# Optimization experiments

Hardware: AMD Instinct MI355X
Metric: run time of the kernel (lower is better)

Reference implementation:

```python
import jax, jax.numpy as jnp
import numpy as np

H = 768; I = 3072; NH = 12; HD = H // NH; L = 2; V = 32000
N = 2048; NSUB = 8; SUBLEN = 256; WIDTH = 512; EPS = 1e-6


def rmsnorm(x, w):
    x32 = x.astype(jnp.float32)
    n = x32 * jax.lax.rsqrt(jnp.mean(x32 * x32, axis=-1, keepdims=True) + EPS)
    return (n * w).astype(x.dtype)


def fixed_pos_embedding(ages, dim):
    # inv_freq: [dim//2]; torch.linspace(0, 2, steps=dim//2)
    inv_freq = 1.0 / (10000.0 ** jnp.linspace(0.0, 2.0, dim // 2))
    t = ages[:, None] * inv_freq[None, :]              # [N, dim//2]
    # stack((s, s), -1).reshape -> duplicate each entry pairwise (interleaved)
    sin = jnp.repeat(jnp.sin(t), 2, axis=-1)[:, None, :]  # [N, 1, dim]
    cos = jnp.repeat(jnp.cos(t), 2, axis=-1)[:, None, :]
    return sin, cos


def apply_rope(x, sin, cos):
    # x: [N, heads, hd]; sin/cos: [N, 1, hd]
    x1 = x[..., 0::2]
    x2 = x[..., 1::2]
    rot = jnp.stack((-x2, x1), axis=-1).reshape(x.shape)
    return x * cos + rot * sin


def build_mask(subject_lengths, n):
    # block-diagonal (per subject) + causal local window of WIDTH
    csum = jnp.cumsum(subject_lengths)
    idx = jnp.arange(n)
    seg = jnp.searchsorted(csum, idx, side='right')   # subject id per token
    i = idx[:, None]; j = idx[None, :]
    same = seg[:, None] == seg[None, :]
    return same & (j <= i) & ((i - j) < WIDTH)        # [N, N] bool


def encoder_layer(x, time_data, sin, cos, mask, norm_w, W_in, W_out):
    h = rmsnorm(x, norm_w)
    all_time = jnp.concatenate((time_data, time_data ** 2), axis=-1)  # [N, 4]
    h = h.at[:, -all_time.shape[1]:].set(all_time.astype(h.dtype))
    t = h @ W_in                                      # [N, 2I + 3H]
    ff = t[:, : 2 * I]
    qkv = t[:, 2 * I:].reshape(-1, 3, NH, HD)
    q = apply_rope(qkv[:, 0], sin, cos)
    k = apply_rope(qkv[:, 1], sin, cos)
    v = qkv[:, 2]
    scores = jnp.einsum('qhd,khd->hqk', q, k) / jnp.sqrt(jnp.float32(HD))
    scores = jnp.where(mask[None, :, :], scores, -jnp.inf)
    probs = jax.nn.softmax(scores, axis=-1)
    attn = jnp.einsum('hqk,khd->qhd', probs, v).reshape(-1, H)
    x1, x2 = jnp.split(ff, 2, axis=-1)
    ffo = jax.nn.silu(x1) * x2                        # swiglu
    return jnp.concatenate((attn, ffo), axis=-1) @ W_out


def setup_inputs() -> dict:
    key = jax.random.key(0)
    ks = jax.random.split(key, 6)
    tokens = jax.random.randint(ks[0], (N,), 0, V)
    ages = jnp.sort(jax.random.uniform(ks[1], (N,), dtype=jnp.float32) * 100.0)
    time_data = jax.random.normal(ks[2], (N, 2), dtype=jnp.float32)
    subject_lengths = jnp.full((NSUB,), SUBLEN, dtype=jnp.int32)
    embed_table = jax.random.normal(ks[3], (V, H), dtype=jnp.float32) * 0.02
    in_norm_w = jnp.ones((H,), jnp.float32)
    out_norm_w = jnp.ones((H,), jnp.float32)
    layer_norm_w = jnp.ones((L, H), jnp.float32)
    layer_Win = jax.random.normal(ks[4], (L, H, 2 * I + 3 * H), dtype=jnp.float32) / np.sqrt(H)
    layer_Wout = jax.random.normal(ks[5], (L, H + I, H), dtype=jnp.float32) / np.sqrt(H + I)
    return dict(tokens=tokens, ages=ages, time_data=time_data,
                subject_lengths=subject_lengths, embed_table=embed_table,
                in_norm_w=in_norm_w, out_norm_w=out_norm_w,
                layer_norm_w=layer_norm_w, layer_Win=layer_Win, layer_Wout=layer_Wout)


def reference(tokens, ages, time_data, subject_lengths, embed_table,
              in_norm_w, out_norm_w, layer_norm_w, layer_Win, layer_Wout):
    x = embed_table[tokens]                           # [N, H]
    x = rmsnorm(x, in_norm_w)
    sin, cos = fixed_pos_embedding(ages, HD)
    mask = build_mask(subject_lengths, x.shape[0])
    for l in range(L):
        x = x + encoder_layer(x, time_data, sin, cos, mask,
                              layer_norm_w[l], layer_Win[l], layer_Wout[l])
    return rmsnorm(x, out_norm_w)
```

## Files before the change

### kernel.cpp

```cpp
#include <hip/hip_runtime.h>
#include <math.h>

typedef unsigned short ushort_t;
typedef float f32x4 __attribute__((ext_vector_type(4)));
typedef __bf16 bf16x8 __attribute__((ext_vector_type(8)));
typedef ushort_t u16x8 __attribute__((ext_vector_type(8)));

#define DEVFN __device__ __forceinline__

DEVFN ushort_t f2bf(float f) {
  unsigned int u = __float_as_uint(f);
  u += 0x7FFFu + ((u >> 16) & 1u);
  return (ushort_t)(u >> 16);
}
DEVFN float bf2f(ushort_t u) { return __uint_as_float((unsigned int)u << 16); }

DEVFN void gload(const ushort_t* src, char* dst) {
  __builtin_amdgcn_global_load_lds(
      (const __attribute__((address_space(1))) unsigned int*)src,
      (__attribute__((address_space(3))) unsigned int*)dst, 16, 0, 0);
}

#define N_TOK  2048
#define HDIM   768
#define TCOLS  8448
#define FFI    3072
#define NHEADS 12
#define HD     64
#define NSEG   8
#define SEGLEN 256
#define ABCOLS 3840
#define KSPLIT 5
#define KCHUNK 768

__global__ void transpose_all(const float* __restrict__ Win, const float* __restrict__ Wout,
                              ushort_t* __restrict__ winT, ushort_t* __restrict__ woutT) {
  __shared__ ushort_t tile[32][33];
  int id = blockIdx.x;
  const float* in; ushort_t* out; int R, C, tr, tc;
  if (id < 12672) {
    const int z = id / 6336; id -= z * 6336;
    R = HDIM; C = TCOLS;
    tc = (id % 264) * 32; tr = (id / 264) * 32;
    in = Win + (size_t)z * R * C; out = winT + (size_t)z * R * C;
  } else {
    id -= 12672;
    const int z = id / 2880; id -= z * 2880;
    R = ABCOLS; C = HDIM;
    tc = (id % 24) * 32; tr = (id / 24) * 32;
    in = Wout + (size_t)z * R * C; out = woutT + (size_t)z * R * C;
  }
  const int tx = threadIdx.x, ty = threadIdx.y;
#pragma unroll
  for (int i = 0; i < 4; ++i)
    tile[ty + i * 8][tx] = f2bf(in[(size_t)(tr + ty + i * 8) * C + tc + tx]);
  __syncthreads();
#pragma unroll
  for (int i = 0; i < 4; ++i)
    out[(size_t)(tc + ty + i * 8) * R + tr + tx] = tile[tx][ty + i * 8];
}

__global__ __launch_bounds__(256) void sincos_kernel(const float* __restrict__ ages,
                                                     float2* __restrict__ sctab) {
  const int n = blockIdx.x * 8 + (threadIdx.x >> 5), k = threadIdx.x & 31;
  const float e = (2.0f * (float)k) / 31.0f;
  const float inv = expf(-e * logf(10000.0f));
  const float t = ages[n] * inv;
  float2 cs; cs.x = cosf(t); cs.y = sinf(t);
  sctab[n * HD + 2 * k] = cs;
  sctab[n * HD + 2 * k + 1] = cs;
}

__global__ __launch_bounds__(256) void rms_init(
    const float* __restrict__ embed, const int* __restrict__ tokens,
    const float* __restrict__ in_nw, const float* __restrict__ layer_nw,
    const float* __restrict__ time_data,
    float* __restrict__ x, ushort_t* __restrict__ hbuf) {
  const int row = blockIdx.x;
  const float* src = embed + (size_t)tokens[row] * HDIM;
  __shared__ float part[4];
  float v[3]; float ss = 0.f;
#pragma unroll
  for (int i = 0; i < 3; ++i) { v[i] = src[threadIdx.x + i * 256]; ss += v[i] * v[i]; }
#pragma unroll
  for (int off = 1; off < 64; off <<= 1) ss += __shfl_xor(ss, off);
  if ((threadIdx.x & 63) == 0) part[threadIdx.x >> 6] = ss;
  __syncthreads();
  const float rs = rsqrtf((part[0] + part[1] + part[2] + part[3]) * (1.0f / HDIM) + 1e-6f);
  float y[3]; float ss2 = 0.f;
#pragma unroll
  for (int i = 0; i < 3; ++i) {
    const int c = threadIdx.x + i * 256;
    y[i] = v[i] * rs * in_nw[c];
    x[(size_t)row * HDIM + c] = y[i];
    ss2 += y[i] * y[i];
  }
#pragma unroll
  for (int off = 1; off < 64; off <<= 1) ss2 += __shfl_xor(ss2, off);
  __syncthreads();
  if ((threadIdx.x & 63) == 0) part[threadIdx.x >> 6] = ss2;
  __syncthreads();
  const float rs2 = rsqrtf((part[0] + part[1] + part[2] + part[3]) * (1.0f / HDIM) + 1e-6f);
#pragma unroll
  for (int i = 0; i < 3; ++i) {
    const int c = threadIdx.x + i * 256;
    float val = y[i] * rs2 * layer_nw[c];
    if (c >= HDIM - 4) {
      const float td = time_data[row * 2 + (c & 1)];
      val = (c >= HDIM - 2) ? td * td : td;
    }
    hbuf[(size_t)row * HDIM + c] = f2bf(val);
  }
}

__global__ __launch_bounds__(256) void rms_fused(
    const float* __restrict__ cpart, float* __restrict__ x,
    const float* __restrict__ w, const float* __restrict__ time_data,
    float* __restrict__ out_f32, ushort_t* __restrict__ out_bf16, const int mode) {
  const int row = blockIdx.x;
  const size_t stride = (size_t)N_TOK * HDIM;
  float v[3]; float ss = 0.f;
#pragma unroll
  for (int i = 0; i < 3; ++i) {
    const size_t idx = (size_t)row * HDIM + threadIdx.x + i * 256;
    float s = x[idx];
#pragma unroll
    for (int z = 0; z < KSPLIT; ++z) s += cpart[z * stride + idx];
    if (mode == 1) x[idx] = s;
    v[i] = s; ss += s * s;
  }
#pragma unroll
  for (int off = 1; off < 64; off <<= 1) ss += __shfl_xor(ss, off);
  __shared__ float part[4];
  if ((threadIdx.x & 63) == 0) part[threadIdx.x >> 6] = ss;
  __syncthreads();
  const float rs = rsqrtf((part[0] + part[1] + part[2] + part[3]) * (1.0f / HDIM) + 1e-6f);
#pragma unroll
  for (int i = 0; i < 3; ++i) {
    const int c = threadIdx.x + i * 256;
    float val = v[i] * rs * w[c];
    if (mode == 1) {
      if (c >= HDIM - 4) {
        const float td = time_data[row * 2 + (c & 1)];
        val = (c >= HDIM - 2) ? td * td : td;
      }
      out_bf16[(size_t)row * HDIM + c] = f2bf(val);
    } else {
      out_f32[(size_t)row * HDIM + c] = val;
    }
  }
}

#define G1_NT 24
#define G1_ABYT 8192
#define G1_BUF  20480

DEVFN int swz64(int p) {
  const int g = ((p >> 6) & 3) ^ ((p >> 8) & 3);
  return p ^ (g << 4);
}
DEVFN int ffmap(int vr) {
  return (vr < 2 * FFI) ? ((((vr >> 4) & 1) * FFI) + ((vr >> 5) << 4) + (vr & 15)) : vr;
}

DEVFN void g1f_stage(const ushort_t* __restrict__ A, const ushort_t* __restrict__ BT,
                     int m0, int n0, int kt_el, char* buf, int tid) {
#pragma unroll
  for (int i = 0; i < 2; ++i) {
    const int q = swz64(i * 4096 + tid * 16);
    gload(A + (size_t)(m0 + (q >> 6)) * HDIM + kt_el + ((q & 63) >> 1),
          buf + i * 4096 + ((tid >> 6) << 10));
  }
#pragma unroll
  for (int i = 0; i < 3; ++i) {
    const int q = swz64(i * 4096 + tid * 16);
    const int vr = n0 + (q >> 6);
    gload(BT + (size_t)ffmap(vr) * HDIM + kt_el + ((q & 63) >> 1),
          buf + G1_ABYT + i * 4096 + ((tid >> 6) << 10));
  }
}

__global__ __launch_bounds__(256, 3) void gemm1f(
    const ushort_t* __restrict__ A, const ushort_t* __restrict__ BT,
    const float2* __restrict__ sctab,
    ushort_t* __restrict__ ab, ushort_t* __restrict__ qr,
    ushort_t* __restrict__ kr, ushort_t* __restrict__ vT) {
  __shared__ __align__(16) char smem[2 * G1_BUF];
  const int tid = threadIdx.x;
  const int l = tid & 63, l15 = l & 15, l4 = l >> 4;
  const int wid = tid >> 6, wr = wid >> 1, wc = wid & 1;
  const int bid = (int)blockIdx.x;
  const int wg = (bid & 7) * 88 + (bid >> 3);
  const int nt = wg >> 4, mt = wg & 15;
  const int m0 = mt * 128, n0 = nt * 192;

  f32x4 acc[4][6] = {};

  g1f_stage(A, BT, m0, n0, 0,  smem, tid);
  g1f_stage(A, BT, m0, n0, 32, smem + G1_BUF, tid);
  asm volatile("s_waitcnt vmcnt(5)" ::: "memory");
  __builtin_amdgcn_s_barrier();
  __builtin_amdgcn_sched_barrier(0);

  for (int t = 0; t < G1_NT; ++t) {
    const char* bufA = smem + (t & 1) * G1_BUF;
    const char* bufB = bufA + G1_ABYT;
    bf16x8 a4[4], b6[6];
#pragma unroll
    for (int m = 0; m < 4; ++m) {
      const int p = (wr * 64 + m * 16 + l15) * 64 + l4 * 16;
      a4[m] = *(const bf16x8*)(bufA + swz64(p));
    }
#pragma unroll
    for (int n = 0; n < 6; ++n) {
      const int p = (wc * 96 + n * 16 + l15) * 64 + l4 * 16;
      b6[n] = *(const bf16x8*)(bufB + swz64(p));
    }
#pragma unroll
    for (int m = 0; m < 4; ++m)
#pragma unroll
      for (int n = 0; n < 6; ++n)
        acc[m][n] = __builtin_amdgcn_mfma_f32_16x16x32_bf16(a4[m], b6[n], acc[m][n], 0, 0, 0);

    if (t == G1_NT - 1) break;
    __builtin_amdgcn_sched_barrier(0);
    __builtin_amdgcn_s_barrier();
    if (t + 2 < G1_NT) {
      g1f_stage(A, BT, m0, n0, (t + 2) * 32, smem + (t & 1) * G1_BUF, tid);
      asm volatile("s_waitcnt vmcnt(5)" ::: "memory");
    } else {
      asm volatile("s_waitcnt vmcnt(0)" ::: "memory");
    }
    __builtin_amdgcn_s_barrier();
    __builtin_amdgcn_sched_barrier(0);
  }

  if (nt < 32) {
#pragma unroll
    for (int m = 0; m < 4; ++m)
#pragma unroll
      for (int np = 0; np < 3; ++np) {
        const int colj = (nt * 6 + wc * 3 + np) * 16 + l15;
#pragma unroll
        for (int r = 0; r < 4; ++r) {
          const float x1 = acc[m][2 * np][r], x2 = acc[m][2 * np + 1][r];
          const float sv = x1 / (1.f + __expf(-x1)) * x2;
          const int row = m0 + wr * 64 + m * 16 + l4 * 4 + r;
          ab[(size_t)row * ABCOLS + HDIM + colj] = f2bf(sv);
        }
      }
  } else {
#pragma unroll
    for (int n = 0; n < 6; ++n) {
      const int gcol = (nt - 32) * 192 + wc * 96 + n * 16;
      const int g = gcol >> 6;
      const int typ = g / NHEADS, h = g - typ * NHEADS;
      const int d = (gcol & 63) + l15;
      if (typ == 2) {
#pragma unroll
        for (int m = 0; m < 4; ++m) {
          ushort4 pk;
          pk.x = f2bf(acc[m][n][0]); pk.y = f2bf(acc[m][n][1]);
          pk.z = f2bf(acc[m][n][2]); pk.w = f2bf(acc[m][n][3]);
          const int row0 = m0 + wr * 64 + m * 16 + l4 * 4;
          *(ushort4*)(vT + ((size_t)h * HD + d) * N_TOK + row0) = pk;
        }
      } else {
        ushort_t* dst = (typ == 0) ? qr : kr;
        const float sgn = (l15 & 1) ? 1.f : -1.f;
#pragma unroll
        for (int m = 0; m < 4; ++m)
#pragma unroll
          for (int r = 0; r < 4; ++r) {
            const float val = acc[m][n][r];
            const float partner = __shfl_xor(val, 1);
            const int row = m0 + wr * 64 + m * 16 + l4 * 4 + r;
            const float2 cs = sctab[row * HD + d];
            dst[((size_t)h * N_TOK + row) * HD + d] = f2bf(val * cs.x + sgn * partner * cs.y);
          }
      }
    }
  }
}

#define G2_NT 12
#define G2_BUF 32768

DEVFN int swz128(int p) { return p ^ (((p >> 7) & 7) << 4); }

DEVFN void g2_stage(const ushort_t* __restrict__ A, const ushort_t* __restrict__ BT,
                    int m0, int n0, int kt_el, char* buf, int tid) {
#pragma unroll
  for (int i = 0; i < 8; ++i) {
    const int p = i * 4096 + tid * 16;
    const bool isA = p < 16384;
    const int q = swz128(isA ? p : p - 16384);
    const int row = q >> 7, colel = (q & 127) >> 1;
    const ushort_t* src = (isA ? A + (size_t)(m0 + row) * ABCOLS
                               : BT + (size_t)(n0 + row) * ABCOLS) + kt_el + colel;
    gload(src, buf + i * 4096 + ((tid >> 6) << 10));
  }
}

__global__ __launch_bounds__(256, 2) void gemm2_splitk(
    const ushort_t* __restrict__ A, const ushort_t* __restrict__ BT,
    float* __restrict__ Cp) {
  __shared__ __align__(16) char smem[2 * G2_BUF];
  const int tid = threadIdx.x;
  const int l = tid & 63, l15 = l & 15, l4 = l >> 4;
  const int w = tid >> 6, wr = w >> 1, wc = w & 1;
  const int m0 = blockIdx.y * 128, n0 = blockIdx.x * 128;
  const int kt0 = blockIdx.z * KCHUNK;

  f32x4 acc[4][4] = {};

  g2_stage(A, BT, m0, n0, kt0, smem, tid);
  g2_stage(A, BT, m0, n0, kt0 + 64, smem + G2_BUF, tid);
  asm volatile("s_waitcnt vmcnt(8)" ::: "memory");
  __builtin_amdgcn_s_barrier();
  __builtin_amdgcn_sched_barrier(0);

  for (int t = 0; t < G2_NT; ++t) {
    const char* bufA = smem + (t & 1) * G2_BUF;
    const char* bufB = bufA + 16384;
    bf16x8 af[4][2], bv[4][2];
#pragma unroll
    for (int kk = 0; kk < 2; ++kk) {
#pragma unroll
      for (int mi = 0; mi < 4; ++mi) {
        const int p = (wr * 64 + mi * 16 + l15) * 128 + kk * 64 + l4 * 16;
        af[mi][kk] = *(const bf16x8*)(bufA + swz128(p));
      }
#pragma unroll
      for (int ni = 0; ni < 4; ++ni) {
        const int p = (wc * 64 + ni * 16 + l15) * 128 + kk * 64 + l4 * 16;
        bv[ni][kk] = *(const bf16x8*)(bufB + swz128(p));
      }
    }
#pragma unroll
    for (int kk = 0; kk < 2; ++kk)
#pragma unroll
      for (int mi = 0; mi < 4; ++mi)
#pragma unroll
        for (int ni = 0; ni < 4; ++ni)
          acc[mi][ni] = __builtin_amdgcn_mfma_f32_16x16x32_bf16(af[mi][kk], bv[ni][kk], acc[mi][ni], 0, 0, 0);

    if (t == G2_NT - 1) break;
    __builtin_amdgcn_sched_barrier(0);
    __builtin_amdgcn_s_barrier();
    if (t + 2 < G2_NT) {
      g2_stage(A, BT, m0, n0, kt0 + (t + 2) * 64, smem + (t & 1) * G2_BUF, tid);
      asm volatile("s_waitcnt vmcnt(8)" ::: "memory");
    } else {
      asm volatile("s_waitcnt vmcnt(0)" ::: "memory");
    }
    __builtin_amdgcn_s_barrier();
    __builtin_amdgcn_sched_barrier(0);
  }

  float* Cz = Cp + (size_t)blockIdx.z * N_TOK * HDIM;
#pragma unroll
  for (int mi = 0; mi < 4; ++mi)
#pragma unroll
    for (int ni = 0; ni < 4; ++ni)
#pragma unroll
      for (int r = 0; r < 4; ++r) {
        const int row = m0 + wr * 64 + mi * 16 + l4 * 4 + r;
        const int col = n0 + wc * 64 + ni * 16 + l15;
        Cz[(size_t)row * HDIM + col] = acc[mi][ni][r];
      }
}

__global__ __launch_bounds__(256) void attn_kernel(
    const ushort_t* __restrict__ qr, const ushort_t* __restrict__ kr,
    const ushort_t* __restrict__ vT, ushort_t* __restrict__ ab) {
  const int h = blockIdx.x, seg = blockIdx.y, z = blockIdx.z;
  const int tid = threadIdx.x;
  const int w = tid >> 6, l = tid & 63;
  const int l15 = l & 15, l4 = l >> 4;
  const int qt = z * 4 + w;
  __shared__ ushort_t P[4][16 * 64];

  const int qrow0 = seg * SEGLEN + qt * 16;
  bf16x8 aq[2];
#pragma unroll
  for (int kk = 0; kk < 2; ++kk)
    aq[kk] = *(const bf16x8*)(qr + ((size_t)h * N_TOK + qrow0 + l15) * HD + kk * 32 + l4 * 8);

  f32x4 o[4] = {};
  float m_run[4], l_run[4];
#pragma unroll
  for (int r = 0; r < 4; ++r) { m_run[r] = -1e30f; l_run[r] = 0.f; }

  const int kbmax = z;
  for (int kb = 0; kb <= kbmax; ++kb) {
    bf16x8 bk[4][2];
#pragma unroll
    for (int ni = 0; ni < 4; ++ni)
#pragma unroll
      for (int kk = 0; kk < 2; ++kk)
        bk[ni][kk] = *(const bf16x8*)(kr + ((size_t)h * N_TOK + seg * SEGLEN + kb * 64 + ni * 16 + l15) * HD + kk * 32 + l4 * 8);
    f32x4 s[4] = {};
#pragma unroll
    for (int ni = 0; ni < 4; ++ni)
#pragma unroll
      for (int kk = 0; kk < 2; ++kk)
        s[ni] = __builtin_amdgcn_mfma_f32_16x16x32_bf16(aq[kk], bk[ni][kk], s[ni], 0, 0, 0);

    const bool diag = (kb == kbmax);
#pragma unroll
    for (int ni = 0; ni < 4; ++ni)
#pragma unroll
      for (int r = 0; r < 4; ++r) {
        float v = s[ni][r] * 0.125f;
        if (diag) {
          const int qrow = qt * 16 + l4 * 4 + r;
          const int jcol = kb * 64 + ni * 16 + l15;
          if (jcol > qrow) v = -1e30f;
        }
        s[ni][r] = v;
      }

    float sc_[4];
#pragma unroll
    for (int r = 0; r < 4; ++r) {
      float pm = fmaxf(fmaxf(s[0][r], s[1][r]), fmaxf(s[2][r], s[3][r]));
      pm = fmaxf(pm, __shfl_xor(pm, 1));
      pm = fmaxf(pm, __shfl_xor(pm, 2));
      pm = fmaxf(pm, __shfl_xor(pm, 4));
      pm = fmaxf(pm, __shfl_xor(pm, 8));
      const float mn = fmaxf(m_run[r], pm);
      sc_[r] = __expf(m_run[r] - mn);
      m_run[r] = mn;
    }
#pragma unroll
    for (int ni = 0; ni < 4; ++ni)
#pragma unroll
      for (int r = 0; r < 4; ++r)
        s[ni][r] = __expf(s[ni][r] - m_run[r]);
#pragma unroll
    for (int r = 0; r < 4; ++r) {
      float ls = s[0][r] + s[1][r] + s[2][r] + s[3][r];
      ls += __shfl_xor(ls, 1);
      ls += __shfl_xor(ls, 2);
      ls += __shfl_xor(ls, 4);
      ls += __shfl_xor(ls, 8);
      l_run[r] = l_run[r] * sc_[r] + ls;
    }
#pragma unroll
    for (int ni = 0; ni < 4; ++ni)
#pragma unroll
      for (int r = 0; r < 4; ++r)
        o[ni][r] *= sc_[r];

#pragma unroll
    for (int ni = 0; ni < 4; ++ni)
#pragma unroll
      for (int r = 0; r < 4; ++r)
        P[w][(l4 * 4 + r) * 64 + ni * 16 + l15] = f2bf(s[ni][r]);

    bf16x8 pa[2], bv[4][2];
#pragma unroll
    for (int k2 = 0; k2 < 2; ++k2)
      pa[k2] = *(const bf16x8*)(&P[w][l15 * 64 + k2 * 32 + l4 * 8]);
#pragma unroll
    for (int ni = 0; ni < 4; ++ni)
#pragma unroll
      for (int k2 = 0; k2 < 2; ++k2)
        bv[ni][k2] = *(const bf16x8*)(vT + ((size_t)h * HD + ni * 16 + l15) * N_TOK + seg * SEGLEN + kb * 64 + k2 * 32 + l4 * 8);
#pragma unroll
    for (int ni = 0; ni < 4; ++ni)
#pragma unroll
      for (int k2 = 0; k2 < 2; ++k2)
        o[ni] = __builtin_amdgcn_mfma_f32_16x16x32_bf16(pa[k2], bv[ni][k2], o[ni], 0, 0, 0);
  }

#pragma unroll
  for (int ni = 0; ni < 4; ++ni)
#pragma unroll
    for (int r = 0; r < 4; ++r) {
      const int row = qrow0 + l4 * 4 + r;
      const int col = h * HD + ni * 16 + l15;
      ab[(size_t)row * ABCOLS + col] = f2bf(o[ni][r] / l_run[r]);
    }
}

extern "C" void kernel_launch(void* const* d_in, const int* in_sizes, int n_in,
                              void* d_out, int out_size, void* d_ws, size_t ws_size,
                              hipStream_t stream) {
  const int*   tokens   = (const int*)d_in[0];
  const float* ages     = (const float*)d_in[1];
  const float* time_d   = (const float*)d_in[2];
  const float* embed    = (const float*)d_in[4];
  const float* in_nw    = (const float*)d_in[5];
  const float* out_nw   = (const float*)d_in[6];
  const float* layer_nw = (const float*)d_in[7];
  const float* Win      = (const float*)d_in[8];
  const float* Wout     = (const float*)d_in[9];
  float* out = (float*)d_out;

  char* ws = (char*)d_ws;
  float*    x      = (float*)   (ws + 0);
  ushort_t* hbuf   = (ushort_t*)(ws + 6291456);
  float2*   sctab  = (float2*)  (ws + 9437184);
  float*    cpart  = (float*)   (ws + 10485760);
  ushort_t* ab     = (ushort_t*)(ws + 41943040);
  ushort_t* qrb    = (ushort_t*)(ws + 57671680);
  ushort_t* krb    = (ushort_t*)(ws + 60817408);
  ushort_t* vTb    = (ushort_t*)(ws + 63963136);
  ushort_t* winT   = (ushort_t*)(ws + 67108864);
  ushort_t* woutT  = (ushort_t*)(ws + 93061120);

  transpose_all<<<dim3(18432), dim3(32, 8), 0, stream>>>(Win, Wout, winT, woutT);
  sincos_kernel<<<dim3(N_TOK / 8), dim3(256), 0, stream>>>(ages, sctab);
  rms_init<<<dim3(N_TOK), dim3(256), 0, stream>>>(embed, tokens, in_nw, layer_nw, time_d,
                                                  x, hbuf);

  for (int lyr = 0; lyr < 2; ++lyr) {
    gemm1f<<<dim3(704), dim3(256), 0, stream>>>(hbuf, winT + (size_t)lyr * TCOLS * HDIM,
                                                sctab, ab, qrb, krb, vTb);
    attn_kernel<<<dim3(NHEADS, NSEG, 4), dim3(256), 0, stream>>>(qrb, krb, vTb, ab);
    gemm2_splitk<<<dim3(HDIM / 128, N_TOK / 128, KSPLIT), dim3(256), 0, stream>>>(
        ab, woutT + (size_t)lyr * HDIM * ABCOLS, cpart);
    if (lyr == 0)
      rms_fused<<<dim3(N_TOK), dim3(256), 0, stream>>>(cpart, x, layer_nw + HDIM, time_d,
                                                       nullptr, hbuf, 1);
    else
      rms_fused<<<dim3(N_TOK), dim3(256), 0, stream>>>(cpart, x, out_nw, nullptr,
                                                       out, nullptr, 2);
  }
}
```

Baseline: 207.0 us.

## Overlap attention with FFN-part split-K GEMM in one fused launch, bf16 partials

```diff
diff --git a/kernel.cpp b/kernel.cpp
--- a/kernel.cpp
+++ b/kernel.cpp
@@ -4,7 +4,6 @@
 typedef unsigned short ushort_t;
 typedef float f32x4 __attribute__((ext_vector_type(4)));
 typedef __bf16 bf16x8 __attribute__((ext_vector_type(8)));
-typedef ushort_t u16x8 __attribute__((ext_vector_type(8)));
 
 #define DEVFN __device__ __forceinline__
 
@@ -30,53 +29,57 @@
 #define NSEG   8
 #define SEGLEN 256
 #define ABCOLS 3840
-#define KSPLIT 5
+#define NPART  6
 #define KCHUNK 768
 
-__global__ void transpose_all(const float* __restrict__ Win, const float* __restrict__ Wout,
-                              ushort_t* __restrict__ winT, ushort_t* __restrict__ woutT) {
-  __shared__ ushort_t tile[32][33];
+__global__ __launch_bounds__(256) void transpose_all(
+    const float* __restrict__ Win, const float* __restrict__ Wout,
+    ushort_t* __restrict__ winT, ushort_t* __restrict__ woutT) {
+  __shared__ ushort_t tile[32][66];
   int id = blockIdx.x;
   const float* in; ushort_t* out; int R, C, tr, tc;
-  if (id < 12672) {
-    const int z = id / 6336; id -= z * 6336;
+  if (id < 6336) {
+    const int z = id / 3168; id -= z * 3168;
     R = HDIM; C = TCOLS;
-    tc = (id % 264) * 32; tr = (id / 264) * 32;
+    tr = (id / 264) * 64; tc = (id % 264) * 32;
     in = Win + (size_t)z * R * C; out = winT + (size_t)z * R * C;
   } else {
-    id -= 12672;
-    const int z = id / 2880; id -= z * 2880;
+    id -= 6336;
+    const int z = id / 1440; id -= z * 1440;
     R = ABCOLS; C = HDIM;
-    tc = (id % 24) * 32; tr = (id / 24) * 32;
+    tr = (id / 24) * 64; tc = (id % 24) * 32;
     in = Wout + (size_t)z * R * C; out = woutT + (size_t)z * R * C;
   }
   const int tx = threadIdx.x, ty = threadIdx.y;
 #pragma unroll
-  for (int i = 0; i < 4; ++i)
-    tile[ty + i * 8][tx] = f2bf(in[(size_t)(tr + ty + i * 8) * C + tc + tx]);
+  for (int i = 0; i < 8; ++i) {
+    const int r = ty + i * 8;
+    tile[tx][r] = f2bf(in[(size_t)(tr + r) * C + tc + tx]);
+  }
   __syncthreads();
 #pragma unroll
-  for (int i = 0; i < 4; ++i)
-    out[(size_t)(tc + ty + i * 8) * R + tr + tx] = tile[tx][ty + i * 8];
-}
-
-__global__ __launch_bounds__(256) void sincos_kernel(const float* __restrict__ ages,
-                                                     float2* __restrict__ sctab) {
-  const int n = blockIdx.x * 8 + (threadIdx.x >> 5), k = threadIdx.x & 31;
-  const float e = (2.0f * (float)k) / 31.0f;
-  const float inv = expf(-e * logf(10000.0f));
-  const float t = ages[n] * inv;
-  float2 cs; cs.x = cosf(t); cs.y = sinf(t);
-  sctab[n * HD + 2 * k] = cs;
-  sctab[n * HD + 2 * k + 1] = cs;
+  for (int i = 0; i < 4; ++i) {
+    const int c = ty + i * 8;
+    ushort2 pk; pk.x = tile[c][2 * tx]; pk.y = tile[c][2 * tx + 1];
+    *(ushort2*)(out + (size_t)(tc + c) * R + tr + 2 * tx) = pk;
+  }
 }
 
 __global__ __launch_bounds__(256) void rms_init(
     const float* __restrict__ embed, const int* __restrict__ tokens,
+    const float* __restrict__ ages,
     const float* __restrict__ in_nw, const float* __restrict__ layer_nw,
     const float* __restrict__ time_data,
-    float* __restrict__ x, ushort_t* __restrict__ hbuf) {
+    float* __restrict__ x, ushort_t* __restrict__ hbuf, float2* __restrict__ sctab) {
   const int row = blockIdx.x;
+  if (threadIdx.x < 32) {
+    const int k = threadIdx.x;
+    const float e = (2.0f * (float)k) / 31.0f;
+    const float t = ages[row] * expf(-e * logf(10000.0f));
+    float2 cs; cs.x = cosf(t); cs.y = sinf(t);
+    sctab[row * HD + 2 * k] = cs;
+    sctab[row * HD + 2 * k + 1] = cs;
+  }
   const float* src = embed + (size_t)tokens[row] * HDIM;
   __shared__ float part[4];
   float v[3]; float ss = 0.f;
@@ -114,7 +117,7 @@
 }
 
 __global__ __launch_bounds__(256) void rms_fused(
-    const float* __restrict__ cpart, float* __restrict__ x,
+    const ushort_t* __restrict__ cpartb, float* __restrict__ x,
     const float* __restrict__ w, const float* __restrict__ time_data,
     float* __restrict__ out_f32, ushort_t* __restrict__ out_bf16, const int mode) {
   const int row = blockIdx.x;
@@ -125,7 +128,7 @@
     const size_t idx = (size_t)row * HDIM + threadIdx.x + i * 256;
     float s = x[idx];
 #pragma unroll
-    for (int z = 0; z < KSPLIT; ++z) s += cpart[z * stride + idx];
+    for (int z = 0; z < NPART; ++z) s += bf2f(cpartb[z * stride + idx]);
     if (mode == 1) x[idx] = s;
     v[i] = s; ss += s * s;
   }
@@ -283,7 +286,6 @@
   }
 }
 
-#define G2_NT 12
 #define G2_BUF 32768
 
 DEVFN int swz128(int p) { return p ^ (((p >> 7) & 7) << 4); }
@@ -302,16 +304,11 @@
   }
 }
 
-__global__ __launch_bounds__(256, 2) void gemm2_splitk(
-    const ushort_t* __restrict__ A, const ushort_t* __restrict__ BT,
-    float* __restrict__ Cp) {
-  __shared__ __align__(16) char smem[2 * G2_BUF];
-  const int tid = threadIdx.x;
+DEVFN void g2_body(const ushort_t* __restrict__ A, const ushort_t* __restrict__ BT,
+                   char* smem, int m0, int n0, int kt0, int NT,
+                   ushort_t* __restrict__ outp, int tid) {
   const int l = tid & 63, l15 = l & 15, l4 = l >> 4;
   const int w = tid >> 6, wr = w >> 1, wc = w & 1;
-  const int m0 = blockIdx.y * 128, n0 = blockIdx.x * 128;
-  const int kt0 = blockIdx.z * KCHUNK;
-
   f32x4 acc[4][4] = {};
 
   g2_stage(A, BT, m0, n0, kt0, smem, tid);
@@ -320,7 +317,7 @@
   __builtin_amdgcn_s_barrier();
   __builtin_amdgcn_sched_barrier(0);
 
-  for (int t = 0; t < G2_NT; ++t) {
+  for (int t = 0; t < NT; ++t) {
     const char* bufA = smem + (t & 1) * G2_BUF;
     const char* bufB = bufA + 16384;
     bf16x8 af[4][2], bv[4][2];
@@ -345,10 +342,10 @@
         for (int ni = 0; ni < 4; ++ni)
           acc[mi][ni] = __builtin_amdgcn_mfma_f32_16x16x32_bf16(af[mi][kk], bv[ni][kk], acc[mi][ni], 0, 0, 0);
 
-    if (t == G2_NT - 1) break;
+    if (t == NT - 1) break;
     __builtin_amdgcn_sched_barrier(0);
     __builtin_amdgcn_s_barrier();
-    if (t + 2 < G2_NT) {
+    if (t + 2 < NT) {
       g2_stage(A, BT, m0, n0, kt0 + (t + 2) * 64, smem + (t & 1) * G2_BUF, tid);
       asm volatile("s_waitcnt vmcnt(8)" ::: "memory");
     } else {
@@ -358,7 +355,6 @@
     __builtin_amdgcn_sched_barrier(0);
   }
 
-  float* Cz = Cp + (size_t)blockIdx.z * N_TOK * HDIM;
 #pragma unroll
   for (int mi = 0; mi < 4; ++mi)
 #pragma unroll
@@ -367,20 +363,13 @@
       for (int r = 0; r < 4; ++r) {
         const int row = m0 + wr * 64 + mi * 16 + l4 * 4 + r;
         const int col = n0 + wc * 64 + ni * 16 + l15;
-        Cz[(size_t)row * HDIM + col] = acc[mi][ni][r];
-      }
-}
-
-__global__ __launch_bounds__(256) void attn_kernel(
-    const ushort_t* __restrict__ qr, const ushort_t* __restrict__ kr,
-    const ushort_t* __restrict__ vT, ushort_t* __restrict__ ab) {
-  const int h = blockIdx.x, seg = blockIdx.y, z = blockIdx.z;
-  const int tid = threadIdx.x;
-  const int w = tid >> 6, l = tid & 63;
-  const int l15 = l & 15, l4 = l >> 4;
-  const int qt = z * 4 + w;
-  __shared__ ushort_t P[4][16 * 64];
-
+        outp[(size_t)row * HDIM + col] = f2bf(acc[mi][ni][r]);
+      }
+}
+
+DEVFN void attn_one(const ushort_t* __restrict__ qr, const ushort_t* __restrict__ kr,
+                    const ushort_t* __restrict__ vT, ushort_t* __restrict__ ab,
+                    int h, int seg, int qt, ushort_t* Pw, int l15, int l4) {
   const int qrow0 = seg * SEGLEN + qt * 16;
   bf16x8 aq[2];
 #pragma unroll
@@ -392,7 +381,7 @@
 #pragma unroll
   for (int r = 0; r < 4; ++r) { m_run[r] = -1e30f; l_run[r] = 0.f; }
 
-  const int kbmax = z;
+  const int kbmax = qt >> 2;
   for (int kb = 0; kb <= kbmax; ++kb) {
     bf16x8 bk[4][2];
 #pragma unroll
@@ -457,12 +446,12 @@
     for (int ni = 0; ni < 4; ++ni)
 #pragma unroll
       for (int r = 0; r < 4; ++r)
-        P[w][(l4 * 4 + r) * 64 + ni * 16 + l15] = f2bf(s[ni][r]);
+        Pw[(l4 * 4 + r) * 64 + ni * 16 + l15] = f2bf(s[ni][r]);
 
     bf16x8 pa[2], bv[4][2];
 #pragma unroll
     for (int k2 = 0; k2 < 2; ++k2)
-      pa[k2] = *(const bf16x8*)(&P[w][l15 * 64 + k2 * 32 + l4 * 8]);
+      pa[k2] = *(const bf16x8*)(&Pw[l15 * 64 + k2 * 32 + l4 * 8]);
 #pragma unroll
     for (int ni = 0; ni < 4; ++ni)
 #pragma unroll
@@ -483,6 +472,44 @@
       const int col = h * HD + ni * 16 + l15;
       ab[(size_t)row * ABCOLS + col] = f2bf(o[ni][r] / l_run[r]);
     }
+}
+
+__global__ __launch_bounds__(256) void fused_mid(
+    const ushort_t* __restrict__ ab, const ushort_t* __restrict__ woutT,
+    ushort_t* __restrict__ cpartb,
+    const ushort_t* __restrict__ qr, const ushort_t* __restrict__ kr,
+    const ushort_t* __restrict__ vT, ushort_t* __restrict__ ab_out) {
+  __shared__ __align__(16) char smem[2 * G2_BUF];
+  const int b = (int)blockIdx.x;
+  const int tid = threadIdx.x;
+  if (b < 192) {
+    const int h = b % NHEADS;
+    const int r2 = b / NHEADS;
+    const int seg = r2 & 7, p = r2 >> 3;
+    const int w = tid >> 6, l = tid & 63;
+    const int l15 = l & 15, l4 = l >> 4;
+    ushort_t* Pw = (ushort_t*)smem + w * (16 * 64);
+    attn_one(qr, kr, vT, ab_out, h, seg, p * 4 + w, Pw, l15, l4);
+    attn_one(qr, kr, vT, ab_out, h, seg, (3 - p) * 4 + w, Pw, l15, l4);
+  } else {
+    const int idx = b - 192;
+    const int z = 1 + (idx / 96);
+    const int rem = idx % 96;
+    const int n0 = (rem % 6) * 128, m0 = (rem / 6) * 128;
+    g2_body(ab, woutT, smem, m0, n0, z * KCHUNK, 12,
+            cpartb + (size_t)(z - 1) * N_TOK * HDIM, tid);
+  }
+}
+
+__global__ __launch_bounds__(256) void gemm2_z0(
+    const ushort_t* __restrict__ ab, const ushort_t* __restrict__ woutT,
+    ushort_t* __restrict__ cpartb) {
+  __shared__ __align__(16) char smem[2 * G2_BUF];
+  const int b = (int)blockIdx.x;
+  const int half = b / 96, rem = b % 96;
+  const int n0 = (rem % 6) * 128, m0 = (rem / 6) * 128;
+  g2_body(ab, woutT, smem, m0, n0, half * 384, 6,
+          cpartb + (size_t)(4 + half) * N_TOK * HDIM, threadIdx.x);
 }
 
 extern "C" void kernel_launch(void* const* d_in, const int* in_sizes, int n_in,
@@ -503,30 +530,30 @@
   float*    x      = (float*)   (ws + 0);
   ushort_t* hbuf   = (ushort_t*)(ws + 6291456);
   float2*   sctab  = (float2*)  (ws + 9437184);
-  float*    cpart  = (float*)   (ws + 10485760);
-  ushort_t* ab     = (ushort_t*)(ws + 41943040);
-  ushort_t* qrb    = (ushort_t*)(ws + 57671680);
-  ushort_t* krb    = (ushort_t*)(ws + 60817408);
-  ushort_t* vTb    = (ushort_t*)(ws + 63963136);
-  ushort_t* winT   = (ushort_t*)(ws + 67108864);
-  ushort_t* woutT  = (ushort_t*)(ws + 93061120);
-
-  transpose_all<<<dim3(18432), dim3(32, 8), 0, stream>>>(Win, Wout, winT, woutT);
-  sincos_kernel<<<dim3(N_TOK / 8), dim3(256), 0, stream>>>(ages, sctab);
-  rms_init<<<dim3(N_TOK), dim3(256), 0, stream>>>(embed, tokens, in_nw, layer_nw, time_d,
-                                                  x, hbuf);
+  ushort_t* cpartb = (ushort_t*)(ws + 10485760);
+  ushort_t* ab     = (ushort_t*)(ws + 29360128);
+  ushort_t* qrb    = (ushort_t*)(ws + 45088768);
+  ushort_t* krb    = (ushort_t*)(ws + 48234496);
+  ushort_t* vTb    = (ushort_t*)(ws + 51380224);
+  ushort_t* winT   = (ushort_t*)(ws + 54525952);
+  ushort_t* woutT  = (ushort_t*)(ws + 80478208);
+
+  transpose_all<<<dim3(9216), dim3(32, 8), 0, stream>>>(Win, Wout, winT, woutT);
+  rms_init<<<dim3(N_TOK), dim3(256), 0, stream>>>(embed, tokens, ages, in_nw, layer_nw,
+                                                  time_d, x, hbuf, sctab);
 
   for (int lyr = 0; lyr < 2; ++lyr) {
     gemm1f<<<dim3(704), dim3(256), 0, stream>>>(hbuf, winT + (size_t)lyr * TCOLS * HDIM,
                                                 sctab, ab, qrb, krb, vTb);
-    attn_kernel<<<dim3(NHEADS, NSEG, 4), dim3(256), 0, stream>>>(qrb, krb, vTb, ab);
-    gemm2_splitk<<<dim3(HDIM / 128, N_TOK / 128, KSPLIT), dim3(256), 0, stream>>>(
-        ab, woutT + (size_t)lyr * HDIM * ABCOLS, cpart);
+    fused_mid<<<dim3(576), dim3(256), 0, stream>>>(ab, woutT + (size_t)lyr * HDIM * ABCOLS,
+                                                   cpartb, qrb, krb, vTb, ab);
+    gemm2_z0<<<dim3(192), dim3(256), 0, stream>>>(ab, woutT + (size_t)lyr * HDIM * ABCOLS,
+                                                  cpartb);
     if (lyr == 0)
-      rms_fused<<<dim3(N_TOK), dim3(256), 0, stream>>>(cpart, x, layer_nw + HDIM, time_d,
+      rms_fused<<<dim3(N_TOK), dim3(256), 0, stream>>>(cpartb, x, layer_nw + HDIM, time_d,
                                                        nullptr, hbuf, 1);
     else
-      rms_fused<<<dim3(N_TOK), dim3(256), 0, stream>>>(cpart, x, out_nw, nullptr,
+      rms_fused<<<dim3(N_TOK), dim3(256), 0, stream>>>(cpartb, x, out_nw, nullptr,
                                                        out, nullptr, 2);
   }
 }
```

Measured after the change: 186.5 us. 9.9% less time.
